# Performance work log

Hardware: AMD Instinct MI355X
Metric: run time of the kernel (lower is better)

Reference implementation:

```python
import jax, jax.numpy as jnp
import numpy as np

EPS = 2.220446049250313e-16  # sys.float_info.epsilon, matches CoCosNet feature_normalize

def feature_normalize(x):
    return x / (jnp.linalg.norm(x, axis=1, keepdims=True) + EPS)

def conv1x1(x, w, b):  # w: (out, in)
    return jnp.einsum('bchw,oc->bohw', x, w) + b[None, :, None, None]

def conv3x3(x, w, b):  # w: (out, in, 3, 3), SAME padding, stride 1
    y = jax.lax.conv_general_dilated(x, w, (1, 1), 'SAME',
                                     dimension_numbers=('NCHW', 'OIHW', 'NCHW'))
    return y + b[None, :, None, None]

@jax.custom_vjp
def sign_sig(x):
    return (x > 0).astype(x.dtype)

def _ss_fwd(x):
    return (x > 0).astype(x.dtype), jax.nn.sigmoid(x)

def _ss_bwd(s, g):
    return (g * s * (1.0 - s),)

sign_sig.defvjp(_ss_fwd, _ss_bwd)

def pono(x, eps=1e-5):  # PositionalNorm2d: normalize over channel dim
    m = jnp.mean(x, axis=1, keepdims=True)
    v = jnp.var(x, axis=1, keepdims=True)
    return (x - m) * jax.lax.rsqrt(v + eps)

def instance_norm(x, eps=1e-5):  # param-free, over spatial dims
    m = jnp.mean(x, axis=(2, 3), keepdims=True)
    v = jnp.var(x, axis=(2, 3), keepdims=True)
    return (x - m) * jax.lax.rsqrt(v + eps)

def setup_inputs() -> dict:
    B, CV, CPOS, H, W = 2, 256, 64, 64, 64
    CQK, DP, IC, NH = CV + CPOS, 64, 3, 128
    key = jax.random.key(0)
    ks = jax.random.split(key, 24)
    n = lambda i, s: jax.random.normal(ks[i], s, jnp.float32)
    w = lambda i, s: n(i, s) * 0.02
    z = lambda s: jnp.zeros(s, jnp.float32)
    return dict(
        q=n(0, (B, CV, H, W)), k=n(1, (B, CV, H, W)), v=n(2, (B, CV, H, W)),
        pos=n(3, (1, CPOS, H, W)),
        seg_map=jax.random.uniform(ks[4], (B, IC, H, W), jnp.float32),
        v2=n(5, (B, CV, H, W)),
        f_w=w(6, (CQK, CQK)), f_b=z(CQK),
        g_w=w(7, (CQK, CQK)), g_b=z(CQK),
        h_w=w(8, (CV, CV)), h_b=z(CV),
        fp_w=w(9, (DP, CQK)), fp_b=z(DP),
        gp_w=w(10, (DP, CQK)), gp_b=z(DP),
        sp_s_w=w(11, (NH, IC, 3, 3)), sp_s_b=z(NH),
        sp_g_w=w(12, (CV, NH, 3, 3)), sp_g_b=z(CV),
        sp_b_w=w(13, (CV, NH, 3, 3)), sp_b_b=z(CV),
        r1_w=w(14, (CV, CV, 3, 3)), r1_b=z(CV),
        r2_w=w(15, (CV, CV, 3, 3)), r2_b=z(CV),
    )

def reference(q, k, v, pos, seg_map, v2,
              f_w, f_b, g_w, g_b, h_w, h_b, fp_w, fp_b, gp_w, gp_b,
              sp_s_w, sp_s_b, sp_g_w, sp_g_b, sp_b_w, sp_b_b,
              r1_w, r1_b, r2_w, r2_b):
    b, cv, h, w = q.shape
    posb = jnp.broadcast_to(pos, (b,) + pos.shape[1:])
    query = jnp.concatenate([feature_normalize(q), posb], axis=1)
    keyt = jnp.concatenate([feature_normalize(k), posb], axis=1)
    qf = conv1x1(query, f_w, f_b)
    kf = conv1x1(keyt, g_w, g_b)
    vh = conv1x1(v, h_w, h_b)
    qp = conv1x1(query, fp_w, fp_b)
    kp = conv1x1(keyt, gp_w, gp_b)
    cqk = qf.shape[1]
    n = h * w
    Q = qf.reshape(b, cqk, n).transpose(0, 2, 1)          # (b, N, c_qk)
    K = kf.reshape(b, cqk, n)                             # (b, c_qk, N)
    V = vh.reshape(b, cv, n).transpose(0, 2, 1)           # (b, N, c_v)
    Qp = qp.reshape(b, -1, n).transpose(0, 2, 1)
    Kp = kp.reshape(b, -1, n)
    mask = sign_sig(jnp.einsum('bnc,bcm->bnm', Qp, Kp) / Kp.shape[1])
    cor = jnp.einsum('bnc,bcm->bnm', Q, K) / jnp.sqrt(jnp.float32(cqk))
    attn = jax.nn.softmax(cor, axis=-1)
    masked = attn * mask
    out = jnp.einsum('bnm,bmc->bnc', masked, V).transpose(0, 2, 1).reshape(b, cv, h, w)
    conf = masked.sum(-1).reshape(b, 1, h, w)
    V2 = v2.reshape(b, -1, n).transpose(0, 2, 1)
    attn2 = jax.nn.softmax(jnp.where(mask > 0, jnp.float32(-10000.0), cor), axis=-1)
    out2 = jnp.einsum('bnm,bmc->bnc', attn2, V2).transpose(0, 2, 1).reshape(b, -1, h, w)
    # SPADE(q, seg_map)
    actv = jax.nn.relu(conv3x3(seg_map, sp_s_w, sp_s_b))
    spade = instance_norm(q) * (1.0 + conv3x3(actv, sp_g_w, sp_g_b)) + conv3x3(actv, sp_b_w, sp_b_b)
    y = pono(out + (1.0 - conf) * spade + q)
    res = y + conv3x3(jax.nn.relu(conv3x3(y, r1_w, r1_b)), r2_w, r2_b)
    return (res, out2, cor)
```

## Files before the change

kernel.cpp:

```cpp
#include <hip/hip_runtime.h>
#include <stdint.h>


#define DEV static __device__ __forceinline__

typedef short short8 __attribute__((ext_vector_type(8)));
typedef float floatx4 __attribute__((ext_vector_type(4)));

DEV float bf2f(unsigned short b) { return __uint_as_float(((unsigned int)b) << 16); }
DEV unsigned short f2bf(float f) {
  unsigned int u = __float_as_uint(f);
  u += 0x7FFFu + ((u >> 16) & 1u);
  return (unsigned short)(u >> 16);
}
DEV float bfround(float f) { return bf2f(f2bf(f)); }

__global__ __launch_bounds__(256)
void cvt_f2b(const float* __restrict__ in, unsigned short* __restrict__ out, int n)
{
  int i = blockIdx.x * 256 + threadIdx.x;
  if (i < n) out[i] = f2bf(in[i]);
}

__global__ __launch_bounds__(256)
void prep_w9(const float* __restrict__ w, unsigned short* __restrict__ w9,
             int CO, int CI)
{
  int i = blockIdx.x * 256 + threadIdx.x;
  int tot = CO * CI * 9;
  if (i >= tot) return;
  int s = i % 9, rest = i / 9;
  int ci = rest % CI, o = rest / CI;
  w9[(long long)o * 9 * CI + s * CI + ci] = f2bf(w[i]);
}

__global__ __launch_bounds__(256)
void colnorm(const float* __restrict__ x, float* __restrict__ rnorm)
{
  int b = blockIdx.y, t = threadIdx.x;
  int n = (blockIdx.x << 5) + (t & 31);
  int cg = t >> 5;
  const float* base = x + ((long long)b << 20) + n;
  float s = 0.f;
#pragma unroll
  for (int c8 = 0; c8 < 32; c8++) {
    float v = base[((long long)(cg * 32 + c8)) << 12];
    s += v * v;
  }
  __shared__ float red[256];
  red[t] = s; __syncthreads();
  for (int st = 128; st >= 32; st >>= 1) {
    if (t < st) red[t] += red[t + st];
    __syncthreads();
  }
  if (t < 32)
    rnorm[(b << 12) + n] = 1.f / (sqrtf(red[t]) + 2.2204460492503131e-16f);
}

__global__ __launch_bounds__(256)
void build_qk3(const float* __restrict__ x, const float* __restrict__ pos,
               const float* __restrict__ rnorm, unsigned short* __restrict__ qt)
{
  __shared__ float tile[64][65];
  int b = blockIdx.z, by = blockIdx.y;
  int n0 = blockIdx.x << 6;
  int tx = threadIdx.x & 63, tg = threadIdx.x >> 6;
  const float* ib;
  int c0;
  if (by < 4) { ib = x + ((long long)b << 20) + ((long long)(by << 6) << 12); c0 = by << 6; }
  else        { ib = pos; c0 = 256; }
#pragma unroll
  for (int i = 0; i < 16; i++) {
    int r = tg * 16 + i;
    tile[r][tx] = ib[((long long)r << 12) + n0 + tx];
  }
  __syncthreads();
#pragma unroll
  for (int i = 0; i < 16; i++) {
    int r = tg * 16 + i;
    float sc = (by < 4) ? rnorm[(b << 12) + n0 + r] : 1.f;
    qt[((long long)(b * 4096 + n0 + r)) * 320 + c0 + tx] = f2bf(tile[tx][r] * sc);
  }
}

__global__ __launch_bounds__(256)
void transpose_c(const float* __restrict__ in, unsigned short* __restrict__ out, int C)
{
  __shared__ float tile[64][65];
  int b = blockIdx.z;
  int c0 = blockIdx.y << 6;
  int n0 = blockIdx.x << 6;
  const float* ib = in + (long long)b * C * 4096;
  unsigned short* ob = out + (long long)b * C * 4096;
  int tx = threadIdx.x & 63, tg = threadIdx.x >> 6;
#pragma unroll
  for (int i = 0; i < 16; i++) {
    int r = tg * 16 + i;
    tile[r][tx] = ib[((long long)(c0 + r) << 12) + n0 + tx];
  }
  __syncthreads();
#pragma unroll
  for (int i = 0; i < 16; i++) {
    int r = tg * 16 + i;
    ob[(long long)(n0 + r) * C + c0 + tx] = f2bf(tile[tx][r]);
  }
}

__global__ __launch_bounds__(256)
void gemm_bt(const unsigned short* __restrict__ A, long long sAb, int lda,
             const unsigned short* __restrict__ Bt, long long sBb, int ldb,
             int Ncols, int K, float alpha,
             const float* __restrict__ bias, int biasMode,
             unsigned short* __restrict__ Cb, long long sCbb, int ldcb,
             float* __restrict__ Cf, long long sCfb, int ldcf,
             unsigned short* __restrict__ Cm)
{
  __shared__ unsigned short As[128][40];
  __shared__ unsigned short Bs[128][40];
  int bz = blockIdx.z;
  const unsigned short* Ab = A + bz * sAb;
  const unsigned short* Bb = Bt + bz * sBb;
  int m0 = blockIdx.y << 7, n0 = blockIdx.x << 7;
  int t = threadIdx.x;
  int lane = t & 63, wave = t >> 6, quad = lane >> 4, l16 = lane & 15;
  int wm = (wave >> 1) << 6, wn = (wave & 1) << 6;

  floatx4 acc[4][4] = {};

  for (int k0 = 0; k0 < K; k0 += 32) {
#pragma unroll
    for (int s = 0; s < 2; s++) {
      int idx = t + (s << 8);
      int row = idx >> 2, ch = (idx & 3) << 3;
      short8 av = *(const short8*)(Ab + (long long)(m0 + row) * lda + k0 + ch);
      *(short8*)&As[row][ch] = av;
      short8 bv = {};
      if (n0 + row < Ncols) bv = *(const short8*)(Bb + (long long)(n0 + row) * ldb + k0 + ch);
      *(short8*)&Bs[row][ch] = bv;
    }
    __syncthreads();
    short8 af[4], bfv[4];
#pragma unroll
    for (int i = 0; i < 4; i++) af[i] = *(const short8*)&As[wm + (i << 4) + l16][quad << 3];
#pragma unroll
    for (int j = 0; j < 4; j++) bfv[j] = *(const short8*)&Bs[wn + (j << 4) + l16][quad << 3];
#pragma unroll
    for (int i = 0; i < 4; i++)
#pragma unroll
      for (int j = 0; j < 4; j++)
        acc[i][j] = __builtin_amdgcn_mfma_f32_16x16x32_bf16(af[i], bfv[j], acc[i][j], 0, 0, 0);
    __syncthreads();
  }

#pragma unroll
  for (int j = 0; j < 4; j++) {
    int col = n0 + wn + (j << 4) + l16;
    if (col >= Ncols) continue;
    float bcol = (biasMode == 1) ? bias[col] : 0.f;
#pragma unroll
    for (int i = 0; i < 4; i++) {
#pragma unroll
      for (int r = 0; r < 4; r++) {
        int row = m0 + wm + (i << 4) + (quad << 2) + r;
        float vv = acc[i][j][r] * alpha + bcol;
        if (biasMode == 2) vv += bias[row];
        if (Cb) Cb[bz * sCbb + (long long)row * ldcb + col] = f2bf(vv);
        if (Cf) Cf[bz * sCfb + (long long)row * ldcf + col] = bfround(vv);
        if (Cm) {
          unsigned long long bal = __ballot(vv > 0.f);
          if (l16 == 0)
            Cm[(long long)bz * 4096 * 256 + (long long)row * 256 + ((n0 + wn + (j << 4)) >> 4)]
              = (unsigned short)(bal >> (quad << 4));
        }
      }
    }
  }
}

__global__ __launch_bounds__(256)
void gemm_conv(const unsigned short* __restrict__ Xt, int CI,
               const unsigned short* __restrict__ W9, int CO,
               const float* __restrict__ bias,
               unsigned short* __restrict__ Cb, int relu,
               float* __restrict__ Cf, const float* __restrict__ addT, int rnd)
{
  __shared__ unsigned short As[128][40];
  __shared__ unsigned short Bs[128][40];
  int bz = blockIdx.z;
  const unsigned short* Xb = Xt + (long long)bz * 4096 * CI;
  int m0 = blockIdx.y << 7, n0 = blockIdx.x << 7;
  int t = threadIdx.x;
  int lane = t & 63, wave = t >> 6, quad = lane >> 4, l16 = lane & 15;
  int wm = (wave >> 1) << 6, wn = (wave & 1) << 6;
  int K9 = 9 * CI;

  floatx4 acc[4][4] = {};

  for (int tap = 0; tap < 9; ++tap) {
    int dy = tap / 3 - 1, dx = tap % 3 - 1;
    int off = dy * 64 + dx;
    for (int kc = 0; kc < CI; kc += 32) {
#pragma unroll
      for (int s = 0; s < 2; s++) {
        int idx = t + (s << 8);
        int row = idx >> 2, ch = (idx & 3) << 3;
        int p = m0 + row;
        int y = (p >> 6) + dy, x = (p & 63) + dx;
        short8 av = {};
        if ((unsigned)y < 64u && (unsigned)x < 64u)
          av = *(const short8*)(Xb + (long long)(p + off) * CI + kc + ch);
        *(short8*)&As[row][ch] = av;
        short8 bv = *(const short8*)(W9 + (long long)(n0 + row) * K9 + tap * CI + kc + ch);
        *(short8*)&Bs[row][ch] = bv;
      }
      __syncthreads();
      short8 af[4], bfv[4];
#pragma unroll
      for (int i = 0; i < 4; i++) af[i] = *(const short8*)&As[wm + (i << 4) + l16][quad << 3];
#pragma unroll
      for (int j = 0; j < 4; j++) bfv[j] = *(const short8*)&Bs[wn + (j << 4) + l16][quad << 3];
#pragma unroll
      for (int i = 0; i < 4; i++)
#pragma unroll
        for (int j = 0; j < 4; j++)
          acc[i][j] = __builtin_amdgcn_mfma_f32_16x16x32_bf16(af[i], bfv[j], acc[i][j], 0, 0, 0);
      __syncthreads();
    }
  }

#pragma unroll
  for (int j = 0; j < 4; j++) {
    int col = n0 + wn + (j << 4) + l16;
    float bcol = bias[col];
#pragma unroll
    for (int i = 0; i < 4; i++) {
#pragma unroll
      for (int r = 0; r < 4; r++) {
        int row = m0 + wm + (i << 4) + (quad << 2) + r;
        float vv = acc[i][j][r] + bcol;
        if (relu) vv = fmaxf(vv, 0.f);
        if (Cb) Cb[((long long)bz * 4096 + row) * CO + col] = f2bf(vv);
        if (Cf) {
          long long oi = ((long long)bz * CO + col) * 4096 + row;
          float ov = vv;
          if (addT) ov += addT[oi];
          Cf[oi] = rnd ? bfround(ov) : ov;
        }
      }
    }
  }
}

__global__ __launch_bounds__(256)
void stats_rows(const float* __restrict__ corF,
                const unsigned char* __restrict__ mbits,
                float4* __restrict__ statA, float* __restrict__ confF)
{
  long long row = blockIdx.x;
  const float4* cr = (const float4*)(corF + (row << 12));
  const unsigned char* mr = mbits + row * 512;
  int t = threadIdx.x;

  float lg[16]; unsigned int mk[16];
#pragma unroll
  for (int i = 0; i < 4; i++) {
    float4 cc = cr[i * 256 + t];
    unsigned char mb = mr[(i * 256 + t) >> 1];
    int sh = (t & 1) << 2;
    lg[4 * i + 0] = cc.x; lg[4 * i + 1] = cc.y;
    lg[4 * i + 2] = cc.z; lg[4 * i + 3] = cc.w;
#pragma unroll
    for (int j = 0; j < 4; j++) mk[4 * i + j] = (mb >> (sh + j)) & 1u;
  }
  float m1 = -3.0e38f, m2 = -3.0e38f; int cnt = 0;
#pragma unroll
  for (int e = 0; e < 16; e++) {
    m1 = fmaxf(m1, lg[e]);
    if (!mk[e]) m2 = fmaxf(m2, lg[e]);
    cnt += (int)mk[e];
  }
  __shared__ float4 red4[256];
  red4[t] = make_float4(m1, m2, 0.f, 0.f); __syncthreads();
  for (int s = 128; s > 0; s >>= 1) {
    if (t < s) {
      red4[t].x = fmaxf(red4[t].x, red4[t + s].x);
      red4[t].y = fmaxf(red4[t].y, red4[t + s].y);
    }
    __syncthreads();
  }
  float rmax1 = red4[0].x;
  float rmax2 = fmaxf(red4[0].y, -10000.f);
  __syncthreads();

  float s1 = 0.f, cn = 0.f, s2 = 0.f;
#pragma unroll
  for (int e = 0; e < 16; e++) {
    float ex = __expf(fminf(lg[e] - rmax1, 0.f));
    s1 += ex;
    if (mk[e]) cn += ex;
    else s2 += __expf(fminf(lg[e] - rmax2, 0.f));
  }
  red4[t] = make_float4(s1, cn, s2, (float)cnt); __syncthreads();
  for (int s = 128; s > 0; s >>= 1) {
    if (t < s) {
      red4[t].x += red4[t + s].x; red4[t].y += red4[t + s].y;
      red4[t].z += red4[t + s].z; red4[t].w += red4[t + s].w;
    }
    __syncthreads();
  }
  if (t == 0) {
    float4 r = red4[0];
    float sum2 = r.z + r.w * __expf(fminf(-10000.f - rmax2, 0.f));
    statA[row] = make_float4(rmax1, 1.f / fmaxf(r.x, 1e-30f),
                             rmax2, 1.f / fmaxf(sum2, 1e-30f));
    confF[row] = r.y / fmaxf(r.x, 1e-30f);
  }
}

__global__ __launch_bounds__(256, 2)
void gemm_pv4(const float* __restrict__ corF,
              const unsigned char* __restrict__ mbits,
              const float4* __restrict__ statA,
              const unsigned short* __restrict__ Bt0,
              const unsigned short* __restrict__ Bt1,
              float* __restrict__ Cf0, float* __restrict__ Cf1)
{
  __shared__ unsigned short As[32][40];
  __shared__ unsigned short Bs[256][40];
  __shared__ float2 sstat[32];
  int bz = blockIdx.y & 1, mode = blockIdx.y >> 1;
  const float* corb = corF + (long long)bz * 4096 * 4096;
  const unsigned char* mbb = mbits + (long long)bz * 4096 * 512;
  const unsigned short* Bb = (mode ? Bt1 : Bt0) + (long long)bz * 256 * 4096;
  int m0 = blockIdx.x << 5;
  int t = threadIdx.x;
  int lane = t & 63, wave = t >> 6, quad = lane >> 4, l16 = lane & 15;
  int wn = wave << 6;
  const float L2E = 1.44269504088896340736f;

  if (t < 32) {
    float4 s = statA[(long long)bz * 4096 + m0 + t];
    float rm = mode ? s.z : s.x, iv = mode ? s.w : s.y;
    sstat[t] = make_float2(-rm * L2E, iv);
  }
  __syncthreads();

  int rA = t >> 3, cA = (t & 7) << 2;
  int rB = t >> 2, cB = (t & 3) << 3;
  float nrmL = sstat[rA].x;
  float mvr = exp2f(-10000.f * L2E + nrmL);

  floatx4 acc[2][4] = {};

  const float* cpb = corb + (long long)(m0 + rA) * 4096 + cA;
  const unsigned char* mbp = mbb + (long long)(m0 + rA) * 512;
  const unsigned short* pbb = Bb + (long long)rB * 4096 + cB;

  float4 pa; short8 pb[4]; unsigned int pmk;
  auto issue = [&](int kk) {
    pa = *(const float4*)(cpb + kk);
    pmk = (unsigned int)(mbp[(kk + cA) >> 3] >> (cA & 7)) & 0xFu;
#pragma unroll
    for (int j = 0; j < 4; j++)
      pb[j] = *(const short8*)(pbb + (long long)(j << 6) * 4096 + kk);
  };

  issue(0);
  for (int k0 = 0; k0 < 4096; k0 += 32) {
    {
      float cs[4] = {pa.x, pa.y, pa.z, pa.w};
      float vs[4];
#pragma unroll
      for (int j = 0; j < 4; j++) {
        float e = exp2f(fmaf(cs[j], L2E, nrmL));
        bool mk = (pmk >> j) & 1u;
        vs[j] = mode ? (mk ? mvr : e) : (mk ? e : 0.f);
      }
      unsigned int u01, u23;
      asm("v_cvt_pk_bf16_f32 %0, %1, %2" : "=v"(u01) : "v"(vs[0]), "v"(vs[1]));
      asm("v_cvt_pk_bf16_f32 %0, %1, %2" : "=v"(u23) : "v"(vs[2]), "v"(vs[3]));
      *(unsigned int*)&As[rA][cA] = u01;
      *(unsigned int*)&As[rA][cA + 2] = u23;
#pragma unroll
      for (int j = 0; j < 4; j++)
        *(short8*)&Bs[rB + (j << 6)][cB] = pb[j];
    }
    __syncthreads();
    if (k0 + 32 < 4096) issue(k0 + 32);
    short8 af[2], bfv[4];
#pragma unroll
    for (int i = 0; i < 2; i++) af[i] = *(const short8*)&As[(i << 4) + l16][quad << 3];
#pragma unroll
    for (int j = 0; j < 4; j++) bfv[j] = *(const short8*)&Bs[wn + (j << 4) + l16][quad << 3];
#pragma unroll
    for (int i = 0; i < 2; i++)
#pragma unroll
      for (int j = 0; j < 4; j++)
        acc[i][j] = __builtin_amdgcn_mfma_f32_16x16x32_bf16(af[i], bfv[j], acc[i][j], 0, 0, 0);
    __syncthreads();
  }

#pragma unroll
  for (int j = 0; j < 4; j++) {
    int col = wn + (j << 4) + l16;
#pragma unroll
    for (int i = 0; i < 2; i++) {
#pragma unroll
      for (int r = 0; r < 4; r++) {
        int lrow = (i << 4) + (quad << 2) + r;
        int row = m0 + lrow;
        float vv = bfround(acc[i][j][r] * sstat[lrow].y);
        if (mode) Cf1[(long long)bz * 256 * 4096 + (long long)col * 4096 + row] = vv;
        else      Cf0[(long long)bz * 4096 * 256 + (long long)row * 256 + col] = vv;
      }
    }
  }
}

__global__ __launch_bounds__(256)
void inorm_stats(const float* __restrict__ q, float* __restrict__ mu, float* __restrict__ rs)
{
  int c = blockIdx.x, b = blockIdx.y, t = threadIdx.x;
  const float* base = q + ((long long)(b * 256 + c) << 12);
  float s = 0.f, s2 = 0.f;
  for (int i = t; i < 4096; i += 256) { float v = base[i]; s += v; s2 += v * v; }
  __shared__ float r1[256], r2[256];
  r1[t] = s; r2[t] = s2; __syncthreads();
  for (int st = 128; st > 0; st >>= 1) {
    if (t < st) { r1[t] += r1[t + st]; r2[t] += r2[t + st]; }
    __syncthreads();
  }
  if (t == 0) {
    float m = r1[0] * (1.f / 4096.f);
    float var = fmaxf(r2[0] * (1.f / 4096.f) - m * m, 0.f);
    mu[b * 256 + c] = m;
    rs[b * 256 + c] = rsqrtf(var + 1e-5f);
  }
}

__global__ __launch_bounds__(256)
void conv3x3(const float* __restrict__ inF,
             const float* __restrict__ wgt, const float* __restrict__ bias,
             int CI, int CO, const float* __restrict__ addF,
             float* __restrict__ outF, int relu, int rnd)
{
  __shared__ float wsm[2304];
  int b = blockIdx.z, o = blockIdx.y, t = threadIdx.x;
  for (int i = t; i < CI * 9; i += 256) wsm[i] = wgt[(long long)o * CI * 9 + i];
  __syncthreads();
  int x = t & 63, y = (blockIdx.x << 2) + (t >> 6);
  bool ym = y > 0, yp = y < 63, xm = x > 0, xp = x < 63;
  int p = y * 64 + x;
  long long ibase = ((long long)b * CI) << 12;
  float acc = bias[o];
  for (int ci = 0; ci < CI; ci++) {
    const float* wp = &wsm[ci * 9];
    long long ib = ibase + ((long long)ci << 12) + p;
    float v00 = (ym && xm) ? inF[ib - 65] : 0.f;
    float v01 = ym ? inF[ib - 64] : 0.f;
    float v02 = (ym && xp) ? inF[ib - 63] : 0.f;
    float v10 = xm ? inF[ib - 1] : 0.f;
    float v11 = inF[ib];
    float v12 = xp ? inF[ib + 1] : 0.f;
    float v20 = (yp && xm) ? inF[ib + 63] : 0.f;
    float v21 = yp ? inF[ib + 64] : 0.f;
    float v22 = (yp && xp) ? inF[ib + 65] : 0.f;
    acc += v00 * wp[0] + v01 * wp[1] + v02 * wp[2]
         + v10 * wp[3] + v11 * wp[4] + v12 * wp[5]
         + v20 * wp[6] + v21 * wp[7] + v22 * wp[8];
  }
  if (relu) acc = fmaxf(acc, 0.f);
  long long oidx = (((long long)(b * CO + o)) << 12) + p;
  if (addF) acc += addF[oidx];
  outF[oidx] = rnd ? bfround(acc) : acc;
}

__global__ __launch_bounds__(256)
void pono_y(const float* __restrict__ outF, const float* __restrict__ confF,
            const float* __restrict__ gF, const float* __restrict__ bF,
            const float* __restrict__ q, const float* __restrict__ mu,
            const float* __restrict__ rs, float* __restrict__ yF,
            unsigned short* __restrict__ yT)
{
  int n = blockIdx.x, b = blockIdx.y, c = threadIdx.x;
  long long cn = ((long long)(b * 256 + c) << 12) + n;
  float qv = q[cn];
  float sp = (qv - mu[b * 256 + c]) * rs[b * 256 + c] * (1.f + gF[cn]) + bF[cn];
  float cf = confF[b * 4096 + n];
  float tv = outF[((long long)(b * 4096 + n) << 8) + c] + (1.f - cf) * sp + qv;
  __shared__ float red[256];
  red[c] = tv; __syncthreads();
  for (int s = 128; s > 0; s >>= 1) { if (c < s) red[c] += red[c + s]; __syncthreads(); }
  float m = red[0] * (1.f / 256.f); __syncthreads();
  float d = tv - m;
  red[c] = d * d; __syncthreads();
  for (int s = 128; s > 0; s >>= 1) { if (c < s) red[c] += red[c + s]; __syncthreads(); }
  float var = fmaxf(red[0] * (1.f / 256.f), 0.f);
  float yv = d * rsqrtf(var + 1e-5f);
  yF[cn] = yv;
  yT[((long long)(b * 4096 + n) << 8) + c] = f2bf(yv);
}


extern "C" void kernel_launch(void* const* d_in, const int* in_sizes, int n_in,
                              void* d_out, int out_size, void* d_ws, size_t ws_size,
                              hipStream_t stream)
{
  (void)in_sizes; (void)n_in; (void)out_size; (void)ws_size;
  const int B = 2, CV = 256, CQK = 320, DP = 64, N = 4096, NH = 128, IC = 3;
  const float INV_SQRT_CQK = 0.05590169943749474241f;

  const float* q    = (const float*)d_in[0];
  const float* k    = (const float*)d_in[1];
  const float* v    = (const float*)d_in[2];
  const float* pos  = (const float*)d_in[3];
  const float* seg  = (const float*)d_in[4];
  const float* v2   = (const float*)d_in[5];
  const float* f_w  = (const float*)d_in[6];
  const float* f_b  = (const float*)d_in[7];
  const float* g_w  = (const float*)d_in[8];
  const float* g_b  = (const float*)d_in[9];
  const float* h_w  = (const float*)d_in[10];
  const float* h_b  = (const float*)d_in[11];
  const float* fp_w = (const float*)d_in[12];
  const float* fp_b = (const float*)d_in[13];
  const float* gp_w = (const float*)d_in[14];
  const float* gp_b = (const float*)d_in[15];
  const float* sp_s_w = (const float*)d_in[16];
  const float* sp_s_b = (const float*)d_in[17];
  const float* sp_g_w = (const float*)d_in[18];
  const float* sp_g_b = (const float*)d_in[19];
  const float* sp_b_w = (const float*)d_in[20];
  const float* sp_b_b = (const float*)d_in[21];
  const float* r1_w = (const float*)d_in[22];
  const float* r1_b = (const float*)d_in[23];
  const float* r2_w = (const float*)d_in[24];
  const float* r2_b = (const float*)d_in[25];

  float* res_o  = (float*)d_out;
  float* out2_o = res_o + (long long)B * CV * N;
  float* cor_o  = res_o + 2ll * B * CV * N;

  unsigned short* query_t = (unsigned short*)cor_o;
  unsigned short* keyt_t  = query_t + (long long)B * N * CQK;
  float*          outBuf  = res_o;

  char* wp_ = (char*)d_ws;
  auto take = [&](size_t bytes) -> void* {
    void* r = wp_; wp_ += (bytes + 255) & ~(size_t)255; return r;
  };
  unsigned short* v_t     = (unsigned short*)take((size_t)B * N * CV * 2);
  unsigned short* qf_t    = (unsigned short*)take((size_t)B * N * CQK * 2);
  unsigned short* kf_t    = (unsigned short*)take((size_t)B * N * CQK * 2);
  unsigned short* qp_t    = (unsigned short*)take((size_t)B * N * DP * 2);
  unsigned short* kp_t    = (unsigned short*)take((size_t)B * N * DP * 2);
  unsigned short* vh      = (unsigned short*)take((size_t)B * CV * N * 2);
  unsigned short* v2b     = (unsigned short*)take((size_t)B * CV * N * 2);
  unsigned short* fwB     = (unsigned short*)take((size_t)CQK * CQK * 2);
  unsigned short* gwB     = (unsigned short*)take((size_t)CQK * CQK * 2);
  unsigned short* fpwB    = (unsigned short*)take((size_t)DP * CQK * 2);
  unsigned short* gpwB    = (unsigned short*)take((size_t)DP * CQK * 2);
  unsigned short* hwB     = (unsigned short*)take((size_t)CV * CV * 2);
  unsigned short* maskB16 = (unsigned short*)take((size_t)B * N * 256 * 2);
  float4*         statA   = (float4*)take((size_t)B * N * 16);
  float*          confF   = (float*)take((size_t)B * N * 4);
  float*          muF     = (float*)take((size_t)B * CV * 4);
  float*          rsF     = (float*)take((size_t)B * CV * 4);
  float*          rnormQ  = (float*)take((size_t)B * N * 4);
  float*          rnormK  = (float*)take((size_t)B * N * 4);
  float*          actv    = (float*)take((size_t)B * NH * N * 4);
  float*          gC      = (float*)take((size_t)B * CV * N * 4);
  float*          bC      = (float*)take((size_t)B * CV * N * 4);
  float*          yF      = (float*)take((size_t)B * CV * N * 4);
  unsigned short* spgW9   = (unsigned short*)take((size_t)CV * 9 * NH * 2);
  unsigned short* spbW9   = (unsigned short*)take((size_t)CV * 9 * NH * 2);
  unsigned short* r1W9    = (unsigned short*)take((size_t)CV * 9 * CV * 2);
  unsigned short* r2W9    = (unsigned short*)take((size_t)CV * 9 * CV * 2);
  unsigned short* yT      = qf_t;
  unsigned short* a1T     = kf_t;
  unsigned short* actvT   = v_t;

  dim3 blk(256);
  auto cvt = [&](const float* in, unsigned short* out, int n) {
    cvt_f2b<<<dim3((n + 255) / 256), blk, 0, stream>>>(in, out, n);
  };
  auto prepw = [&](const float* w, unsigned short* w9, int CO, int CI) {
    prep_w9<<<dim3((CO * CI * 9 + 255) / 256), blk, 0, stream>>>(w, w9, CO, CI);
  };
  auto gemm = [&](const unsigned short* A, long long sAb, int lda,
                  const unsigned short* Bt, long long sBb, int ldb,
                  int M, int Nc, int K, float alpha,
                  const float* bias, int biasMode,
                  unsigned short* Cb, long long sCbb, int ldcb,
                  float* Cf, long long sCfb, int ldcf,
                  unsigned short* Cm) {
    dim3 grid((Nc + 127) / 128, M / 128, B);
    gemm_bt<<<grid, blk, 0, stream>>>(A, sAb, lda, Bt, sBb, ldb, Nc, K, alpha,
                                      bias, biasMode, Cb, sCbb, ldcb,
                                      Cf, sCfb, ldcf, Cm);
  };
  auto conv = [&](const unsigned short* Xt, int CI, const unsigned short* W9,
                  const float* bias, unsigned short* Cb, int relu,
                  float* Cf, const float* addT, int rnd) {
    gemm_conv<<<dim3(CV / 128, N / 128, B), blk, 0, stream>>>(
        Xt, CI, W9, CV, bias, Cb, relu, Cf, addT, rnd);
  };

  cvt(f_w, fwB, CQK * CQK);
  cvt(g_w, gwB, CQK * CQK);
  cvt(fp_w, fpwB, DP * CQK);
  cvt(gp_w, gpwB, DP * CQK);
  cvt(h_w, hwB, CV * CV);
  cvt(v2, v2b, B * CV * N);
  prepw(sp_g_w, spgW9, CV, NH);
  prepw(sp_b_w, spbW9, CV, NH);
  prepw(r1_w, r1W9, CV, CV);
  prepw(r2_w, r2W9, CV, CV);

  colnorm<<<dim3(128, B), blk, 0, stream>>>(q, rnormQ);
  colnorm<<<dim3(128, B), blk, 0, stream>>>(k, rnormK);
  build_qk3<<<dim3(64, 5, B), blk, 0, stream>>>(q, pos, rnormQ, query_t);
  build_qk3<<<dim3(64, 5, B), blk, 0, stream>>>(k, pos, rnormK, keyt_t);
  transpose_c<<<dim3(64, 4, B), blk, 0, stream>>>(v, v_t, CV);

  gemm(query_t, (long long)N * CQK, CQK, fwB, 0, CQK, N, CQK, CQK, 1.f, f_b, 1,
       qf_t, (long long)N * CQK, CQK, nullptr, 0, 0, nullptr);
  gemm(keyt_t, (long long)N * CQK, CQK, gwB, 0, CQK, N, CQK, CQK, 1.f, g_b, 1,
       kf_t, (long long)N * CQK, CQK, nullptr, 0, 0, nullptr);
  gemm(query_t, (long long)N * CQK, CQK, fpwB, 0, CQK, N, DP, CQK, 1.f, fp_b, 1,
       qp_t, (long long)N * DP, DP, nullptr, 0, 0, nullptr);
  gemm(keyt_t, (long long)N * CQK, CQK, gpwB, 0, CQK, N, DP, CQK, 1.f, gp_b, 1,
       kp_t, (long long)N * DP, DP, nullptr, 0, 0, nullptr);
  gemm(hwB, 0, CV, v_t, (long long)N * CV, CV, CV, N, CV, 1.f, h_b, 2,
       vh, (long long)CV * N, N, nullptr, 0, 0, nullptr);

  gemm(qf_t, (long long)N * CQK, CQK, kf_t, (long long)N * CQK, CQK, N, N, CQK,
       INV_SQRT_CQK, nullptr, 0, nullptr, 0, 0,
       cor_o, (long long)N * N, N, nullptr);
  gemm(qp_t, (long long)N * DP, DP, kp_t, (long long)N * DP, DP, N, N, DP, 1.f,
       nullptr, 0, nullptr, 0, 0, nullptr, 0, 0, maskB16);

  stats_rows<<<dim3(B * N), blk, 0, stream>>>(cor_o, (const unsigned char*)maskB16,
                                              statA, confF);
  gemm_pv4<<<dim3(128, 2 * B), blk, 0, stream>>>(
      cor_o, (const unsigned char*)maskB16, statA, vh, v2b, outBuf, out2_o);

  inorm_stats<<<dim3(CV, B), blk, 0, stream>>>(q, muF, rsF);
  conv3x3<<<dim3(16, NH, B), blk, 0, stream>>>(seg, sp_s_w, sp_s_b, IC, NH, nullptr, actv, 1, 0);
  transpose_c<<<dim3(64, 2, B), blk, 0, stream>>>(actv, actvT, NH);
  conv(actvT, NH, spgW9, sp_g_b, nullptr, 0, gC, nullptr, 0);
  conv(actvT, NH, spbW9, sp_b_b, nullptr, 0, bC, nullptr, 0);
  pono_y<<<dim3(N, B), blk, 0, stream>>>(outBuf, confF, gC, bC, q, muF, rsF, yF, yT);
  conv(yT, CV, r1W9, r1_b, a1T, 1, nullptr, nullptr, 0);
  conv(a1T, CV, r2W9, r2_b, nullptr, 0, res_o, yF, 1);
}
```

Baseline: 825.3 us.

## Load PV B-operand directly into registers and double-buffer A tile in LDS

The attention-times-V GEMM kernel no longer stages the V/V2 operand through shared memory. Each wave now loads its MFMA B fragments straight from global memory into registers. The A tile (exp of cor with mask applied) is double-buffered in LDS, and the loop is unrolled by two so loads for the next step are issued ahead. This removes LDS traffic for B and one barrier per step, but it adds register pressure and makes the global B loads less coalesced (16-byte per-lane row-strided reads).

```diff
diff --git a/kernel.cpp b/kernel.cpp
--- a/kernel.cpp
+++ b/kernel.cpp
@@ -318,15 +318,14 @@
 }
 
 __global__ __launch_bounds__(256, 2)
-void gemm_pv4(const float* __restrict__ corF,
+void gemm_pv5(const float* __restrict__ corF,
               const unsigned char* __restrict__ mbits,
               const float4* __restrict__ statA,
               const unsigned short* __restrict__ Bt0,
               const unsigned short* __restrict__ Bt1,
               float* __restrict__ Cf0, float* __restrict__ Cf1)
 {
-  __shared__ unsigned short As[32][40];
-  __shared__ unsigned short Bs[256][40];
+  __shared__ unsigned short As[2][32][40];
   __shared__ float2 sstat[32];
   int bz = blockIdx.y & 1, mode = blockIdx.y >> 1;
   const float* corb = corF + (long long)bz * 4096 * 4096;
@@ -346,7 +345,6 @@
   __syncthreads();
 
   int rA = t >> 3, cA = (t & 7) << 2;
-  int rB = t >> 2, cB = (t & 3) << 3;
   float nrmL = sstat[rA].x;
   float mvr = exp2f(-10000.f * L2E + nrmL);
 
@@ -354,50 +352,60 @@
 
   const float* cpb = corb + (long long)(m0 + rA) * 4096 + cA;
   const unsigned char* mbp = mbb + (long long)(m0 + rA) * 512;
-  const unsigned short* pbb = Bb + (long long)rB * 4096 + cB;
-
-  float4 pa; short8 pb[4]; unsigned int pmk;
-  auto issue = [&](int kk) {
+  const unsigned short* pbb = Bb + (long long)(wn + l16) * 4096 + (quad << 3);
+
+  float4 paA, paB; unsigned int mkA, mkB;
+  short8 pbA[4], pbB[4];
+
+  auto issueA = [&](int kk, float4& pa, unsigned int& pmk) {
     pa = *(const float4*)(cpb + kk);
     pmk = (unsigned int)(mbp[(kk + cA) >> 3] >> (cA & 7)) & 0xFu;
+  };
+  auto issueB = [&](int kk, short8* pb) {
 #pragma unroll
     for (int j = 0; j < 4; j++)
-      pb[j] = *(const short8*)(pbb + (long long)(j << 6) * 4096 + kk);
-  };
-
-  issue(0);
-  for (int k0 = 0; k0 < 4096; k0 += 32) {
-    {
-      float cs[4] = {pa.x, pa.y, pa.z, pa.w};
-      float vs[4];
-#pragma unroll
-      for (int j = 0; j < 4; j++) {
-        float e = exp2f(fmaf(cs[j], L2E, nrmL));
-        bool mk = (pmk >> j) & 1u;
-        vs[j] = mode ? (mk ? mvr : e) : (mk ? e : 0.f);
-      }
-      unsigned int u01, u23;
-      asm("v_cvt_pk_bf16_f32 %0, %1, %2" : "=v"(u01) : "v"(vs[0]), "v"(vs[1]));
-      asm("v_cvt_pk_bf16_f32 %0, %1, %2" : "=v"(u23) : "v"(vs[2]), "v"(vs[3]));
-      *(unsigned int*)&As[rA][cA] = u01;
-      *(unsigned int*)&As[rA][cA + 2] = u23;
+      pb[j] = *(const short8*)(pbb + (long long)(j << 4) * 4096 + kk);
+  };
+  auto commit = [&](int p, float4 pa, unsigned int pmk) {
+    float cs[4] = {pa.x, pa.y, pa.z, pa.w};
+    float vs[4];
+#pragma unroll
+    for (int j = 0; j < 4; j++) {
+      float e = exp2f(fmaf(cs[j], L2E, nrmL));
+      bool mk = (pmk >> j) & 1u;
+      vs[j] = mode ? (mk ? mvr : e) : (mk ? e : 0.f);
+    }
+    unsigned int u01, u23;
+    asm("v_cvt_pk_bf16_f32 %0, %1, %2" : "=v"(u01) : "v"(vs[0]), "v"(vs[1]));
+    asm("v_cvt_pk_bf16_f32 %0, %1, %2" : "=v"(u23) : "v"(vs[2]), "v"(vs[3]));
+    *(unsigned int*)&As[p][rA][cA] = u01;
+    *(unsigned int*)&As[p][rA][cA + 2] = u23;
+  };
+  auto mma = [&](int p, const short8* pb) {
+    short8 af[2];
+#pragma unroll
+    for (int i = 0; i < 2; i++) af[i] = *(const short8*)&As[p][(i << 4) + l16][quad << 3];
+#pragma unroll
+    for (int i = 0; i < 2; i++)
 #pragma unroll
       for (int j = 0; j < 4; j++)
-        *(short8*)&Bs[rB + (j << 6)][cB] = pb[j];
-    }
-    __syncthreads();
-    if (k0 + 32 < 4096) issue(k0 + 32);
-    short8 af[2], bfv[4];
-#pragma unroll
-    for (int i = 0; i < 2; i++) af[i] = *(const short8*)&As[(i << 4) + l16][quad << 3];
-#pragma unroll
-    for (int j = 0; j < 4; j++) bfv[j] = *(const short8*)&Bs[wn + (j << 4) + l16][quad << 3];
-#pragma unroll
-    for (int i = 0; i < 2; i++)
-#pragma unroll
-      for (int j = 0; j < 4; j++)
-        acc[i][j] = __builtin_amdgcn_mfma_f32_16x16x32_bf16(af[i], bfv[j], acc[i][j], 0, 0, 0);
-    __syncthreads();
+        acc[i][j] = __builtin_amdgcn_mfma_f32_16x16x32_bf16(af[i], pb[j], acc[i][j], 0, 0, 0);
+  };
+
+  issueA(0, paA, mkA); issueB(0, pbA);
+  issueA(32, paB, mkB); issueB(32, pbB);
+
+  for (int k0 = 0; k0 < 4096; k0 += 64) {
+    commit(0, paA, mkA);
+    if (k0 + 64 < 4096) issueA(k0 + 64, paA, mkA);
+    __syncthreads();
+    mma(0, pbA);
+    if (k0 + 64 < 4096) issueB(k0 + 64, pbA);
+    commit(1, paB, mkB);
+    if (k0 + 96 < 4096) issueA(k0 + 96, paB, mkB);
+    __syncthreads();
+    mma(1, pbB);
+    if (k0 + 96 < 4096) issueB(k0 + 96, pbB);
   }
 
 #pragma unroll
@@ -642,7 +650,7 @@
 
   stats_rows<<<dim3(B * N), blk, 0, stream>>>(cor_o, (const unsigned char*)maskB16,
                                               statA, confF);
-  gemm_pv4<<<dim3(128, 2 * B), blk, 0, stream>>>(
+  gemm_pv5<<<dim3(128, 2 * B), blk, 0, stream>>>(
       cor_o, (const unsigned char*)maskB16, statA, vh, v2b, outBuf, out2_o);
 
   inorm_stats<<<dim3(CV, B), blk, 0, stream>>>(q, muF, rsF);
```

Measured after the change: 848.4 us. +2.8%, slower.
